# Optimization experiments

Hardware: AMD Instinct MI355X
Metric: run time of the kernel (lower is better)

## Reference

```python
import jax, jax.numpy as jnp
import numpy as np
import math

B, T, S, C, W = 32, 512, 128, 30, 10  # batch, seq, spans, candidates, max span width
D_CTX, D_ENT, H, V = 768, 300, 100, 200000
EPS = 1e-5
NEG = -1e30


def layer_norm(x, g, b):
    mu = jnp.mean(x, axis=-1, keepdims=True)
    var = jnp.mean((x - mu) ** 2, axis=-1, keepdims=True)
    return (x - mu) / jnp.sqrt(var + EPS) * g + b


def setup_inputs() -> dict:
    key = jax.random.key(0)
    ks = jax.random.split(key, 12)
    contextual_embeddings = jax.random.normal(ks[0], (B, T, D_CTX), jnp.float32)
    mask = jnp.ones((B, T), jnp.int32)
    starts = jax.random.randint(ks[1], (B, S), 0, T - W)
    widths = jax.random.randint(ks[2], (B, S), 0, W)
    ends = starts + widths  # inclusive end, AllenNLP convention
    # pad last 8 spans per example with -1 to exercise span masking
    pad = jnp.arange(S)[None, :] >= S - 8
    starts = jnp.where(pad, -1, starts)
    ends = jnp.where(pad, -1, ends)
    candidate_spans = jnp.stack([starts, ends], axis=-1)
    candidate_entities = jax.random.randint(ks[3], (B, S, C), 1, V)
    pri = jax.random.uniform(ks[4], (B, S, C), jnp.float32)
    candidate_entity_priors = pri / pri.sum(-1, keepdims=True)
    candidate_segment_ids = jnp.zeros((B, S, C), jnp.int32)
    # parameters
    entity_table = jax.random.normal(ks[5], (V, D_ENT), jnp.float32) * 0.02
    proj_W = jax.random.normal(ks[6], (D_ENT, D_CTX), jnp.float32) * 0.02
    proj_b = jnp.zeros((D_ENT,), jnp.float32)
    kg_g = jnp.ones((D_ENT,), jnp.float32)
    kg_b = jnp.zeros((D_ENT,), jnp.float32)
    ln_g = jnp.ones((D_ENT,), jnp.float32)
    ln_b = jnp.zeros((D_ENT,), jnp.float32)
    attn_W = jax.random.normal(ks[7], (1, D_ENT), jnp.float32) * 0.02
    attn_b = jnp.zeros((1,), jnp.float32)
    W1 = jax.random.normal(ks[8], (H, 2), jnp.float32) * 0.02
    b1 = jnp.zeros((H,), jnp.float32)
    W2 = jax.random.normal(ks[9], (1, H), jnp.float32) * 0.02
    b2 = jnp.zeros((1,), jnp.float32)
    return dict(contextual_embeddings=contextual_embeddings, mask=mask,
                candidate_spans=candidate_spans, candidate_entities=candidate_entities,
                candidate_entity_priors=candidate_entity_priors,
                candidate_segment_ids=candidate_segment_ids,
                entity_table=entity_table, proj_W=proj_W, proj_b=proj_b,
                kg_g=kg_g, kg_b=kg_b, ln_g=ln_g, ln_b=ln_b,
                attn_W=attn_W, attn_b=attn_b, W1=W1, b1=b1, W2=W2, b2=b2)


def reference(contextual_embeddings, mask, candidate_spans, candidate_entities,
              candidate_entity_priors, candidate_segment_ids, entity_table,
              proj_W, proj_b, kg_g, kg_b, ln_g, ln_b, attn_W, attn_b,
              W1, b1, W2, b2):
    # --- entity embedding lookup + KG layer norm ---
    ent_emb = layer_norm(entity_table[candidate_entities], kg_g, kg_b)  # (B,S,C,D)

    # --- bert -> kg projection ---
    proj = contextual_embeddings @ proj_W.T + proj_b  # (B,T,D_ENT)

    span_mask = candidate_spans[:, :, 0] > -1  # (B,S)

    # --- SelfAttentiveSpanExtractor ---
    att_logits = (proj @ attn_W.T + attn_b)[..., 0]  # (B,T)
    starts = candidate_spans[..., 0]
    ends = candidate_spans[..., 1]
    widths = ends - starts
    offs = jnp.arange(W)  # max span width
    idx = starts[..., None] + offs  # (B,S,W)
    valid = (offs <= widths[..., None]) & (idx >= 0) & (idx < T)
    idx_c = jnp.where(valid, idx, 0)
    idx_flat = idx_c.reshape(B, S * W)
    span_emb = jnp.take_along_axis(proj, idx_flat[..., None], axis=1).reshape(B, S, W, D_ENT)
    span_log = jnp.take_along_axis(att_logits, idx_flat, axis=1).reshape(B, S, W)
    attn = jax.nn.softmax(jnp.where(valid, span_log, NEG), axis=-1)  # (B,S,W)
    span_rep = jnp.einsum('bsw,bswd->bsd', attn, span_emb)
    span_rep = span_rep * span_mask[..., None].astype(span_rep.dtype)
    span_rep = layer_norm(span_rep, ln_g, ln_b)  # (B,S,D)

    # --- DotAttentionWithPrior ---
    scores = jnp.einsum('bsd,bscd->bsc', span_rep, ent_emb) / math.sqrt(D_ENT)
    feat = jnp.stack([scores, candidate_entity_priors], axis=-1)  # (B,S,C,2)
    h = jax.nn.relu(feat @ W1.T + b1)
    link = (h @ W2.T + b2)[..., 0]  # (B,S,C)
    entity_mask = candidate_entities > 0
    linking_scores = jnp.where(entity_mask, link, -10000.0)
    normed = jax.nn.softmax(linking_scores, axis=-1)
    weighted = jnp.einsum('bsc,bscd->bsd', normed, ent_emb)
    return linking_scores, weighted
```

## Files before the change

kernel.cpp:

```cpp
#include <hip/hip_runtime.h>
#include <hip/hip_bf16.h>
#include <math.h>

#define BB 32
#define TT 512
#define SS 128
#define CC 30
#define WW 10
#define DCTX 768
#define DENT 300
#define HH 100
#define EPSF 1e-5f
#define NEGF -1e30f

typedef __attribute__((ext_vector_type(8))) short bf16x8;
typedef __attribute__((ext_vector_type(4))) float f32x4;

#define NK  (DCTX / 32)
#define NCT 20

template<int C, int M>
__device__ __forceinline__ float dppadd(float x) {
    union { float f; int i; } u, r;
    u.f = x;
    r.i = __builtin_amdgcn_update_dpp(0, u.i, C, M, 0xf, true);
    return x + r.f;
}
__device__ __forceinline__ float wave_red(float x) {
    x = dppadd<0x111, 0xf>(x);
    x = dppadd<0x112, 0xf>(x);
    x = dppadd<0x114, 0xf>(x);
    x = dppadd<0x118, 0xf>(x);
    x = dppadd<0x142, 0xa>(x);
    x = dppadd<0x143, 0xc>(x);
    union { float f; int i; } u; u.f = x;
    u.i = __builtin_amdgcn_readlane(u.i, 63);
    return u.f;
}

__device__ __forceinline__ ushort f2bf(float f) {
    __hip_bfloat16 h = __float2bfloat16(f);
    return *reinterpret_cast<ushort*>(&h);
}

__device__ __forceinline__ float dot4(float4 a, float4 b) {
    return a.x*b.x + a.y*b.y + a.z*b.z + a.w*b.w;
}
__device__ __forceinline__ float hadd8(float4 a, float4 b) {
    return a.x+a.y+a.z+a.w + b.x+b.y+b.z+b.w;
}
__device__ __forceinline__ ushort4 cvt4(float4 v) {
    ushort4 h; h.x = f2bf(v.x); h.y = f2bf(v.y); h.z = f2bf(v.z); h.w = f2bf(v.w);
    return h;
}

__global__ __launch_bounds__(256) void wpre_kernel(
    const float* __restrict__ Wt, ushort* __restrict__ wpre)
{
    const int g = blockIdx.x * 256 + threadIdx.x;
    const int l = g & 63;
    const int t = (g >> 6) % NK;
    const int ct = g / (NK * 64);
    const int col = ct * 16 + (l & 15);
    const int k = t * 32 + (l >> 4) * 8;
    ushort4 h0 = {0, 0, 0, 0}, h1 = {0, 0, 0, 0};
    if (col < DENT) {
        h0 = cvt4(*(const float4*)(Wt + (size_t)col * DCTX + k));
        h1 = cvt4(*(const float4*)(Wt + (size_t)col * DCTX + k + 4));
    }
    *(ushort4*)(wpre + (size_t)g * 8)     = h0;
    *(ushort4*)(wpre + (size_t)g * 8 + 4) = h1;
}

#define GBM 64
#define LDA 40

__global__ __launch_bounds__(512) void gemm_proj_mfma(
    const float*  __restrict__ A,
    const ushort* __restrict__ wpre,
    const float*  __restrict__ bias,
    float* __restrict__ out)
{
    __shared__ ushort Al[2][GBM * LDA];
    const int tid = threadIdx.x;
    const int lane = tid & 63;
    const int wv = tid >> 6;
    const int wm = wv >> 2;
    const int wn = wv & 3;
    const int m0 = blockIdx.x * GBM;
    const int ar = tid >> 3;
    const int ak = (tid & 7) * 4;
    const int lr = lane & 15;
    const int kq = (lane >> 4) * 8;

    const float* aP = A + (size_t)(m0 + ar) * DCTX + ak;
    const ushort* bp = wpre + (size_t)wn * 5 * NK * 512 + (size_t)lane * 8;

    f32x4 acc[2][5];
    #pragma unroll
    for (int i = 0; i < 2; ++i)
        #pragma unroll
        for (int j = 0; j < 5; ++j)
            acc[i][j] = (f32x4){0.f, 0.f, 0.f, 0.f};

    bf16x8 cb[5], nb[5];
    #pragma unroll
    for (int j = 0; j < 5; ++j)
        cb[j] = *(const bf16x8*)(bp + (size_t)j * NK * 512);

#define STOREA(BUF, v_) (*(ushort4*)&Al[BUF][ar * LDA + ak] = cvt4(v_))

#define COMPUTE(BUF) do {                                                      \
        bf16x8 af_[2];                                                         \
        _Pragma("unroll")                                                      \
        for (int i_ = 0; i_ < 2; ++i_)                                         \
            af_[i_] = *(const bf16x8*)&Al[BUF][(wm*32 + i_*16 + lr)*LDA + kq]; \
        _Pragma("unroll")                                                      \
        for (int j_ = 0; j_ < 5; ++j_)                                         \
            acc[0][j_] = __builtin_amdgcn_mfma_f32_16x16x32_bf16(              \
                af_[0], cb[j_], acc[0][j_], 0, 0, 0);                          \
        _Pragma("unroll")                                                      \
        for (int j_ = 0; j_ < 5; ++j_)                                         \
            acc[1][j_] = __builtin_amdgcn_mfma_f32_16x16x32_bf16(              \
                af_[1], cb[j_], acc[1][j_], 0, 0, 0);                          \
    } while (0)

    float4 avA = *(const float4*)(aP);
    float4 avB = *(const float4*)(aP + 32);
    STOREA(0, avA);
    __syncthreads();

    #pragma unroll 1
    for (int kk = 0; kk < NK; kk += 2) {
        #pragma unroll
        for (int j = 0; j < 5; ++j)
            nb[j] = *(const bf16x8*)(bp + ((size_t)j * NK + kk + 1) * 512);
        if (kk + 2 < NK) avA = *(const float4*)(aP + (kk + 2) * 32);
        COMPUTE(0);
        STOREA(1, avB);
        __syncthreads();
        #pragma unroll
        for (int j = 0; j < 5; ++j) cb[j] = nb[j];
        if (kk + 2 < NK) {
            #pragma unroll
            for (int j = 0; j < 5; ++j)
                nb[j] = *(const bf16x8*)(bp + ((size_t)j * NK + kk + 2) * 512);
            avB = *(const float4*)(aP + (kk + 3) * 32);
        }
        COMPUTE(1);
        if (kk + 2 < NK) STOREA(0, avA);
        __syncthreads();
        #pragma unroll
        for (int j = 0; j < 5; ++j) cb[j] = nb[j];
    }

    const int lq = lane >> 4;
    #pragma unroll
    for (int j = 0; j < 5; ++j) {
        int col = wn * 80 + j * 16 + lr;
        if (col < DENT) {
            float bv = bias[col];
            #pragma unroll
            for (int i = 0; i < 2; ++i)
                #pragma unroll
                for (int r = 0; r < 4; ++r) {
                    int row = m0 + wm * 32 + i * 16 + lq * 4 + r;
                    out[(size_t)row * DENT + col] = acc[i][j][r] + bv;
                }
        }
    }
}

__global__ __launch_bounds__(256) void span_kernel(
    const float* __restrict__ proj,
    const int*   __restrict__ spans,
    const float* __restrict__ attn_W,
    const float* __restrict__ attn_b,
    const float* __restrict__ ln_g,
    const float* __restrict__ ln_b,
    const float* __restrict__ kg_g,
    const float* __restrict__ kg_b,
    float* __restrict__ srg_out,
    float* __restrict__ sgsb)
{
    const int bs = blockIdx.x * 4 + (threadIdx.x >> 6);
    const int b = bs >> 7;
    const int lane = threadIdx.x & 63;
    const int start = spans[bs * 2 + 0];
    const int end   = spans[bs * 2 + 1];
    const int width = end - start;
    const bool lo = lane < 11;
    const float4 z = make_float4(0.f, 0.f, 0.f, 0.f);

    const float4* attW4 = (const float4*)attn_W;
    float4 w0 = attW4[lane];
    float4 w1 = lo ? attW4[64 + lane] : z;

    float4 a0[WW], a1[WW];
    float slog[WW];
    bool vld[WW];
    #pragma unroll
    for (int w = 0; w < WW; ++w) {
        int idx = start + w;
        vld[w] = (w <= width) && (idx >= 0) && (idx < TT);
        const float4* pr = (const float4*)(proj + (size_t)(b * TT + (vld[w] ? idx : 0)) * DENT);
        a0[w] = pr[lane];
        a1[w] = lo ? pr[64 + lane] : z;
        slog[w] = dot4(a0[w], w0) + dot4(a1[w], w1);
    }
    const float ab = attn_b[0];
    #pragma unroll
    for (int w = 0; w < WW; ++w) {
        float r = wave_red(slog[w]);
        slog[w] = vld[w] ? r + ab : NEGF;
    }
    float m = slog[0];
    #pragma unroll
    for (int w = 1; w < WW; ++w) m = fmaxf(m, slog[w]);
    float den = 0.f;
    float aw[WW];
    #pragma unroll
    for (int w = 0; w < WW; ++w) { aw[w] = expf(slog[w] - m); den += aw[w]; }
    const float inv = 1.f / den;
    const float msk = (start > -1) ? inv : 0.f;

    float4 acc0 = z, acc1 = z;
    #pragma unroll
    for (int w = 0; w < WW; ++w) {
        float c = aw[w] * msk;
        acc0.x = fmaf(c, a0[w].x, acc0.x); acc0.y = fmaf(c, a0[w].y, acc0.y);
        acc0.z = fmaf(c, a0[w].z, acc0.z); acc0.w = fmaf(c, a0[w].w, acc0.w);
        acc1.x = fmaf(c, a1[w].x, acc1.x); acc1.y = fmaf(c, a1[w].y, acc1.y);
        acc1.z = fmaf(c, a1[w].z, acc1.z); acc1.w = fmaf(c, a1[w].w, acc1.w);
    }
    float s1 = wave_red(hadd8(acc0, acc1));
    float s2 = wave_red(dot4(acc0, acc0) + dot4(acc1, acc1));
    const float mu = s1 * (1.f / DENT);
    const float rstd = rsqrtf(s2 * (1.f / DENT) - mu * mu + EPSF);

    const float4* lg4 = (const float4*)ln_g;  const float4* lb4 = (const float4*)ln_b;
    const float4* gg4 = (const float4*)kg_g;  const float4* gb4 = (const float4*)kg_b;
    float pg = 0.f, pb = 0.f;
    float4* so = (float4*)(srg_out + (size_t)bs * DENT);
    {
        float4 g = lg4[lane], bb_ = lb4[lane], gg = gg4[lane], gb = gb4[lane];
        float4 val;
        val.x = fmaf((acc0.x - mu) * rstd, g.x, bb_.x);
        val.y = fmaf((acc0.y - mu) * rstd, g.y, bb_.y);
        val.z = fmaf((acc0.z - mu) * rstd, g.z, bb_.z);
        val.w = fmaf((acc0.w - mu) * rstd, g.w, bb_.w);
        float4 vg = make_float4(val.x * gg.x, val.y * gg.y, val.z * gg.z, val.w * gg.w);
        so[lane] = vg;
        pg += vg.x + vg.y + vg.z + vg.w;
        pb += val.x * gb.x + val.y * gb.y + val.z * gb.z + val.w * gb.w;
    }
    if (lo) {
        float4 g = lg4[64 + lane], bb_ = lb4[64 + lane], gg = gg4[64 + lane], gb = gb4[64 + lane];
        float4 val;
        val.x = fmaf((acc1.x - mu) * rstd, g.x, bb_.x);
        val.y = fmaf((acc1.y - mu) * rstd, g.y, bb_.y);
        val.z = fmaf((acc1.z - mu) * rstd, g.z, bb_.z);
        val.w = fmaf((acc1.w - mu) * rstd, g.w, bb_.w);
        float4 vg = make_float4(val.x * gg.x, val.y * gg.y, val.z * gg.z, val.w * gg.w);
        so[64 + lane] = vg;
        pg += vg.x + vg.y + vg.z + vg.w;
        pb += val.x * gb.x + val.y * gb.y + val.z * gb.z + val.w * gb.w;
    }
    pg = wave_red(pg);
    pb = wave_red(pb);
    if (lane == 0) { sgsb[bs * 2 + 0] = pg; sgsb[bs * 2 + 1] = pb; }
}

__global__ __launch_bounds__(512) void final_fused(
    const float* __restrict__ srg,
    const float* __restrict__ sgsb,
    const int*   __restrict__ cand,
    const float* __restrict__ priors,
    const float* __restrict__ table,
    const float* __restrict__ W1,
    const float* __restrict__ b1,
    const float* __restrict__ W2,
    const float* __restrict__ b2,
    const float* __restrict__ kg_g,
    const float* __restrict__ kg_b,
    float* __restrict__ out_link,
    float* __restrict__ out_w)
{
    __shared__ float rows[CC][DENT];
    __shared__ float smu[CC], srs[CC], ssc[CC], sexp[CC];
    const int bs = blockIdx.x;
    const int tid = threadIdx.x;
    const int lane = tid & 63;
    const int wv = tid >> 6;
    const bool lo = lane < 11;
    const float4 z = make_float4(0.f, 0.f, 0.f, 0.f);

    const int c0 = wv, c1 = wv + 8, c2 = wv + 16, c3 = wv + 24;
    const bool has3 = (c3 < CC);
    const int e0 = cand[bs * CC + c0];
    const int e1 = cand[bs * CC + c1];
    const int e2 = cand[bs * CC + c2];
    const int e3 = has3 ? cand[bs * CC + c3] : e2;

    const float4* r0 = (const float4*)(table + (size_t)e0 * DENT);
    const float4* r1 = (const float4*)(table + (size_t)e1 * DENT);
    const float4* r2 = (const float4*)(table + (size_t)e2 * DENT);
    const float4* r3 = (const float4*)(table + (size_t)e3 * DENT);
    float4 xa0 = r0[lane], xa1 = r1[lane], xa2 = r2[lane], xa3 = r3[lane];
    float4 xb0 = lo ? r0[64 + lane] : z;
    float4 xb1 = lo ? r1[64 + lane] : z;
    float4 xb2 = lo ? r2[64 + lane] : z;
    float4 xb3 = lo ? r3[64 + lane] : z;

    const float4* sg4 = (const float4*)(srg + (size_t)bs * DENT);
    float4 g0 = sg4[lane];
    float4 g1 = lo ? sg4[64 + lane] : z;
    const float SG = sgsb[bs * 2 + 0];
    const float SB = sgsb[bs * 2 + 1];

    const float W1a0 = W1[2 * lane], W1b0 = W1[2 * lane + 1];
    const float B10 = b1[lane], W20 = W2[lane];
    float W1a1 = 0.f, W1b1 = 0.f, B11 = 0.f, W21 = 0.f;
    if (lane < HH - 64) {
        int j = lane + 64;
        W1a1 = W1[2 * j]; W1b1 = W1[2 * j + 1]; B11 = b1[j]; W21 = W2[j];
    }
    const float b2v = b2[0];
    const float p0 = priors[bs * CC + c0];
    const float p1 = priors[bs * CC + c1];
    const float p2 = priors[bs * CC + c2];
    const float p3 = has3 ? priors[bs * CC + c3] : 0.f;

    *(float4*)&rows[c0][lane * 4] = xa0;
    *(float4*)&rows[c1][lane * 4] = xa1;
    *(float4*)&rows[c2][lane * 4] = xa2;
    if (has3) *(float4*)&rows[c3][lane * 4] = xa3;
    if (lo) {
        *(float4*)&rows[c0][256 + lane * 4] = xb0;
        *(float4*)&rows[c1][256 + lane * 4] = xb1;
        *(float4*)&rows[c2][256 + lane * 4] = xb2;
        if (has3) *(float4*)&rows[c3][256 + lane * 4] = xb3;
    }

    float s1_0 = wave_red(hadd8(xa0, xb0));
    float s1_1 = wave_red(hadd8(xa1, xb1));
    float s1_2 = wave_red(hadd8(xa2, xb2));
    float s1_3 = wave_red(hadd8(xa3, xb3));
    float s2_0 = wave_red(dot4(xa0, xa0) + dot4(xb0, xb0));
    float s2_1 = wave_red(dot4(xa1, xa1) + dot4(xb1, xb1));
    float s2_2 = wave_red(dot4(xa2, xa2) + dot4(xb2, xb2));
    float s2_3 = wave_red(dot4(xa3, xa3) + dot4(xb3, xb3));
    float s3_0 = wave_red(dot4(g0, xa0) + dot4(g1, xb0));
    float s3_1 = wave_red(dot4(g0, xa1) + dot4(g1, xb1));
    float s3_2 = wave_red(dot4(g0, xa2) + dot4(g1, xb2));
    float s3_3 = wave_red(dot4(g0, xa3) + dot4(g1, xb3));
    const float isd = rsqrtf((float)DENT);

#define CAND_TAIL(K, CK, EK, PK)                                               \
    do {                                                                       \
        float mu_ = s1_##K * (1.f / DENT);                                     \
        float rstd_ = rsqrtf(s2_##K * (1.f / DENT) - mu_ * mu_ + EPSF);        \
        float score_ = (rstd_ * (s3_##K - mu_ * SG) + SB) * isd;               \
        float h_ = fmaxf(fmaf(W1a0, score_, fmaf(W1b0, PK, B10)), 0.f);        \
        float h2_ = fmaxf(fmaf(W1a1, score_, fmaf(W1b1, PK, B11)), 0.f);       \
        float lp_ = fmaf(W21, h2_, W20 * h_);                                  \
        lp_ = wave_red(lp_) + b2v;                                             \
        float link_ = (EK > 0) ? lp_ : -10000.0f;                              \
        if (lane == 0) {                                                       \
            smu[CK] = mu_; srs[CK] = rstd_; ssc[CK] = link_;                   \
            out_link[bs * CC + CK] = link_;                                    \
        }                                                                      \
    } while (0)

    CAND_TAIL(0, c0, e0, p0);
    CAND_TAIL(1, c1, e1, p1);
    CAND_TAIL(2, c2, e2, p2);
    if (has3) CAND_TAIL(3, c3, e3, p3);
    __syncthreads();

    if (tid < CC) {
        float m = ssc[0];
        #pragma unroll
        for (int c = 1; c < CC; ++c) m = fmaxf(m, ssc[c]);
        sexp[tid] = expf(ssc[tid] - m);
    }
    __syncthreads();

    const int d = tid;
    if (d < DENT) {
        float den = 0.f;
        #pragma unroll
        for (int c = 0; c < CC; ++c) den += sexp[c];
        const float inv = 1.f / den;
        float acc = 0.f, S2 = 0.f, sn = 0.f;
        #pragma unroll
        for (int c = 0; c < CC; ++c) {
            float n = sexp[c] * inv;
            float coef = n * srs[c];
            acc = fmaf(coef, rows[c][d], acc);
            S2 = fmaf(coef, smu[c], S2);
            sn += n;
        }
        out_w[(size_t)bs * DENT + d] = kg_g[d] * (acc - S2) + kg_b[d] * sn;
    }
}

extern "C" void kernel_launch(void* const* d_in, const int* in_sizes, int n_in,
                              void* d_out, int out_size, void* d_ws, size_t ws_size,
                              hipStream_t stream) {
    const float* ctx    = (const float*)d_in[0];
    const int*   spans  = (const int*)d_in[2];
    const int*   cand   = (const int*)d_in[3];
    const float* priors = (const float*)d_in[4];
    const float* table  = (const float*)d_in[6];
    const float* projW  = (const float*)d_in[7];
    const float* projb  = (const float*)d_in[8];
    const float* kg_g   = (const float*)d_in[9];
    const float* kg_b   = (const float*)d_in[10];
    const float* ln_g   = (const float*)d_in[11];
    const float* ln_b   = (const float*)d_in[12];
    const float* attW   = (const float*)d_in[13];
    const float* attb   = (const float*)d_in[14];
    const float* W1     = (const float*)d_in[15];
    const float* b1     = (const float*)d_in[16];
    const float* W2     = (const float*)d_in[17];
    const float* b2     = (const float*)d_in[18];

    float* proj = (float*)d_ws;
    float* srg  = proj + (size_t)BB * TT * DENT;
    float* sgsb = srg + (size_t)BB * SS * DENT;
    ushort* wpre = (ushort*)srg;

    float* out_link = (float*)d_out;
    float* out_w    = out_link + (size_t)BB * SS * CC;

    wpre_kernel<<<NCT * NK * 64 / 256, 256, 0, stream>>>(projW, wpre);
    gemm_proj_mfma<<<BB * TT / GBM, 512, 0, stream>>>(ctx, wpre, projb, proj);
    span_kernel<<<BB * SS / 4, 256, 0, stream>>>(proj, spans, attW, attb,
                                                 ln_g, ln_b, kg_g, kg_b, srg, sgsb);
    final_fused<<<BB * SS, 512, 0, stream>>>(srg, sgsb, cand, priors, table,
                                             W1, b1, W2, b2, kg_g, kg_b,
                                             out_link, out_w);
}
```

Before: 82.14 us.

## Split final fused kernel into per-candidate score kernel and weighted-sum kernel

The final kernel is split in two. A score kernel runs one wave per (span, candidate) and writes per-candidate stats (mean, rstd, link) to the workspace. A weighted kernel then recomputes the softmax per span and re-gathers the entity table rows directly from global memory rather than staging them in LDS. This is meant to spread the gather and reduction work over more blocks for better parallelism, at the cost of an extra launch, reading the entity rows twice, and a stats array written over the start of the proj workspace.

```diff
diff --git a/kernel.cpp b/kernel.cpp
--- a/kernel.cpp
+++ b/kernel.cpp
@@ -271,7 +271,7 @@
     if (lane == 0) { sgsb[bs * 2 + 0] = pg; sgsb[bs * 2 + 1] = pb; }
 }
 
-__global__ __launch_bounds__(512) void final_fused(
+__global__ __launch_bounds__(256) void score_kernel(
     const float* __restrict__ srg,
     const float* __restrict__ sgsb,
     const int*   __restrict__ cand,
@@ -281,36 +281,24 @@
     const float* __restrict__ b1,
     const float* __restrict__ W2,
     const float* __restrict__ b2,
-    const float* __restrict__ kg_g,
-    const float* __restrict__ kg_b,
-    float* __restrict__ out_link,
-    float* __restrict__ out_w)
+    float*  __restrict__ out_link,
+    float4* __restrict__ stats)
 {
-    __shared__ float rows[CC][DENT];
-    __shared__ float smu[CC], srs[CC], ssc[CC], sexp[CC];
-    const int bs = blockIdx.x;
-    const int tid = threadIdx.x;
-    const int lane = tid & 63;
-    const int wv = tid >> 6;
+    const int lane = threadIdx.x & 63;
+    const int wv = threadIdx.x >> 6;
+    const int bs = blockIdx.x >> 3;
+    const int cg = blockIdx.x & 7;
+    const int c  = cg * 4 + wv;
+    const bool act = c < CC;
+    const int q = bs * CC + (act ? c : 0);
     const bool lo = lane < 11;
     const float4 z = make_float4(0.f, 0.f, 0.f, 0.f);
 
-    const int c0 = wv, c1 = wv + 8, c2 = wv + 16, c3 = wv + 24;
-    const bool has3 = (c3 < CC);
-    const int e0 = cand[bs * CC + c0];
-    const int e1 = cand[bs * CC + c1];
-    const int e2 = cand[bs * CC + c2];
-    const int e3 = has3 ? cand[bs * CC + c3] : e2;
-
-    const float4* r0 = (const float4*)(table + (size_t)e0 * DENT);
-    const float4* r1 = (const float4*)(table + (size_t)e1 * DENT);
-    const float4* r2 = (const float4*)(table + (size_t)e2 * DENT);
-    const float4* r3 = (const float4*)(table + (size_t)e3 * DENT);
-    float4 xa0 = r0[lane], xa1 = r1[lane], xa2 = r2[lane], xa3 = r3[lane];
-    float4 xb0 = lo ? r0[64 + lane] : z;
-    float4 xb1 = lo ? r1[64 + lane] : z;
-    float4 xb2 = lo ? r2[64 + lane] : z;
-    float4 xb3 = lo ? r3[64 + lane] : z;
+    const int e = cand[q];
+    const float prior = priors[q];
+    const float4* row = (const float4*)(table + (size_t)e * DENT);
+    float4 xa = row[lane];
+    float4 xb = lo ? row[64 + lane] : z;
 
     const float4* sg4 = (const float4*)(srg + (size_t)bs * DENT);
     float4 g0 = sg4[lane];
@@ -326,58 +314,44 @@
         W1a1 = W1[2 * j]; W1b1 = W1[2 * j + 1]; B11 = b1[j]; W21 = W2[j];
     }
     const float b2v = b2[0];
-    const float p0 = priors[bs * CC + c0];
-    const float p1 = priors[bs * CC + c1];
-    const float p2 = priors[bs * CC + c2];
-    const float p3 = has3 ? priors[bs * CC + c3] : 0.f;
-
-    *(float4*)&rows[c0][lane * 4] = xa0;
-    *(float4*)&rows[c1][lane * 4] = xa1;
-    *(float4*)&rows[c2][lane * 4] = xa2;
-    if (has3) *(float4*)&rows[c3][lane * 4] = xa3;
-    if (lo) {
-        *(float4*)&rows[c0][256 + lane * 4] = xb0;
-        *(float4*)&rows[c1][256 + lane * 4] = xb1;
-        *(float4*)&rows[c2][256 + lane * 4] = xb2;
-        if (has3) *(float4*)&rows[c3][256 + lane * 4] = xb3;
-    }
-
-    float s1_0 = wave_red(hadd8(xa0, xb0));
-    float s1_1 = wave_red(hadd8(xa1, xb1));
-    float s1_2 = wave_red(hadd8(xa2, xb2));
-    float s1_3 = wave_red(hadd8(xa3, xb3));
-    float s2_0 = wave_red(dot4(xa0, xa0) + dot4(xb0, xb0));
-    float s2_1 = wave_red(dot4(xa1, xa1) + dot4(xb1, xb1));
-    float s2_2 = wave_red(dot4(xa2, xa2) + dot4(xb2, xb2));
-    float s2_3 = wave_red(dot4(xa3, xa3) + dot4(xb3, xb3));
-    float s3_0 = wave_red(dot4(g0, xa0) + dot4(g1, xb0));
-    float s3_1 = wave_red(dot4(g0, xa1) + dot4(g1, xb1));
-    float s3_2 = wave_red(dot4(g0, xa2) + dot4(g1, xb2));
-    float s3_3 = wave_red(dot4(g0, xa3) + dot4(g1, xb3));
-    const float isd = rsqrtf((float)DENT);
-
-#define CAND_TAIL(K, CK, EK, PK)                                               \
-    do {                                                                       \
-        float mu_ = s1_##K * (1.f / DENT);                                     \
-        float rstd_ = rsqrtf(s2_##K * (1.f / DENT) - mu_ * mu_ + EPSF);        \
-        float score_ = (rstd_ * (s3_##K - mu_ * SG) + SB) * isd;               \
-        float h_ = fmaxf(fmaf(W1a0, score_, fmaf(W1b0, PK, B10)), 0.f);        \
-        float h2_ = fmaxf(fmaf(W1a1, score_, fmaf(W1b1, PK, B11)), 0.f);       \
-        float lp_ = fmaf(W21, h2_, W20 * h_);                                  \
-        lp_ = wave_red(lp_) + b2v;                                             \
-        float link_ = (EK > 0) ? lp_ : -10000.0f;                              \
-        if (lane == 0) {                                                       \
-            smu[CK] = mu_; srs[CK] = rstd_; ssc[CK] = link_;                   \
-            out_link[bs * CC + CK] = link_;                                    \
-        }                                                                      \
-    } while (0)
-
-    CAND_TAIL(0, c0, e0, p0);
-    CAND_TAIL(1, c1, e1, p1);
-    CAND_TAIL(2, c2, e2, p2);
-    if (has3) CAND_TAIL(3, c3, e3, p3);
+
+    float s1 = wave_red(hadd8(xa, xb));
+    float s2 = wave_red(dot4(xa, xa) + dot4(xb, xb));
+    float s3 = wave_red(dot4(g0, xa) + dot4(g1, xb));
+
+    const float mu = s1 * (1.f / DENT);
+    const float rstd = rsqrtf(s2 * (1.f / DENT) - mu * mu + EPSF);
+    const float score = (rstd * (s3 - mu * SG) + SB) * rsqrtf((float)DENT);
+
+    float h  = fmaxf(fmaf(W1a0, score, fmaf(W1b0, prior, B10)), 0.f);
+    float h2 = fmaxf(fmaf(W1a1, score, fmaf(W1b1, prior, B11)), 0.f);
+    float lp = wave_red(fmaf(W21, h2, W20 * h)) + b2v;
+    const float link = (e > 0) ? lp : -10000.0f;
+
+    if (act && lane == 0) {
+        out_link[q] = link;
+        stats[q] = make_float4(mu, rstd, link, 0.f);
+    }
+}
+
+__global__ __launch_bounds__(320) void weighted_kernel(
+    const int*    __restrict__ cand,
+    const float4* __restrict__ stats,
+    const float*  __restrict__ table,
+    const float*  __restrict__ kg_g,
+    const float*  __restrict__ kg_b,
+    float* __restrict__ out_w)
+{
+    __shared__ float ssc[CC], smu[CC], srs[CC], sexp[CC];
+    __shared__ int sid[CC];
+    const int bs = blockIdx.x;
+    const int tid = threadIdx.x;
+    if (tid < CC) {
+        float4 st = stats[bs * CC + tid];
+        smu[tid] = st.x; srs[tid] = st.y; ssc[tid] = st.z;
+        sid[tid] = cand[bs * CC + tid];
+    }
     __syncthreads();
-
     if (tid < CC) {
         float m = ssc[0];
         #pragma unroll
@@ -392,15 +366,19 @@
         #pragma unroll
         for (int c = 0; c < CC; ++c) den += sexp[c];
         const float inv = 1.f / den;
-        float acc = 0.f, S2 = 0.f, sn = 0.f;
+        float coef[CC];
+        float S2 = 0.f, sn = 0.f;
         #pragma unroll
         for (int c = 0; c < CC; ++c) {
             float n = sexp[c] * inv;
-            float coef = n * srs[c];
-            acc = fmaf(coef, rows[c][d], acc);
-            S2 = fmaf(coef, smu[c], S2);
+            coef[c] = n * srs[c];
+            S2 = fmaf(coef[c], smu[c], S2);
             sn += n;
         }
+        float acc = 0.f;
+        #pragma unroll
+        for (int c = 0; c < CC; ++c)
+            acc = fmaf(coef[c], table[(size_t)sid[c] * DENT + d], acc);
         out_w[(size_t)bs * DENT + d] = kg_g[d] * (acc - S2) + kg_b[d] * sn;
     }
 }
@@ -430,6 +408,7 @@
     float* srg  = proj + (size_t)BB * TT * DENT;
     float* sgsb = srg + (size_t)BB * SS * DENT;
     ushort* wpre = (ushort*)srg;
+    float4* stats = (float4*)d_ws;
 
     float* out_link = (float*)d_out;
     float* out_w    = out_link + (size_t)BB * SS * CC;
@@ -438,7 +417,7 @@
     gemm_proj_mfma<<<BB * TT / GBM, 512, 0, stream>>>(ctx, wpre, projb, proj);
     span_kernel<<<BB * SS / 4, 256, 0, stream>>>(proj, spans, attW, attb,
                                                  ln_g, ln_b, kg_g, kg_b, srg, sgsb);
-    final_fused<<<BB * SS, 512, 0, stream>>>(srg, sgsb, cand, priors, table,
-                                             W1, b1, W2, b2, kg_g, kg_b,
-                                             out_link, out_w);
-}
+    score_kernel<<<BB * SS * 8, 256, 0, stream>>>(srg, sgsb, cand, priors, table,
+                                                  W1, b1, W2, b2, out_link, stats);
+    weighted_kernel<<<BB * SS, 320, 0, stream>>>(cand, stats, table, kg_g, kg_b, out_w);
+}
```

After: 111.5 us. 1.36x slower.
